# Kernel optimization log

Hardware: AMD Instinct MI355X
Metric: run time of the kernel (lower is better)

Reference implementation:

```python
import jax, jax.numpy as jnp
import numpy as np

N_PER_GROUP = 64
INPUT_DIM = 512
BATCH = 16384


def setup_inputs() -> dict:
    key = jax.random.key(0)
    k1, k2, k3 = jax.random.split(key, 3)
    x = jax.random.normal(k1, (BATCH, INPUT_DIM), dtype=jnp.float32)
    # xavier-uniform-ish prototypes
    prototype_vectors = jax.random.normal(k2, (2, N_PER_GROUP, INPUT_DIM), dtype=jnp.float32) * 0.05
    # mixture_fn = Linear(2*d, d)
    W_mix = jax.random.normal(k3, (INPUT_DIM, 2 * INPUT_DIM), dtype=jnp.float32) * (1.0 / np.sqrt(2 * INPUT_DIM))
    b_mix = jnp.zeros((INPUT_DIM,), dtype=jnp.float32)
    return {"x": x, "prototype_vectors": prototype_vectors, "W_mix": W_mix, "b_mix": b_mix}


def _mixed_prototypes(prototype_vectors, W_mix, b_mix):
    # Batched replacement of the nested j,l Python loop:
    # pair (j,l) -> concat(proto[0,j], proto[1,l]) -> Linear(2d -> d)
    n, d = prototype_vectors.shape[1], prototype_vectors.shape[2]
    g0 = jnp.broadcast_to(prototype_vectors[0][:, None, :], (n, n, d))  # [j,l,d]
    g1 = jnp.broadcast_to(prototype_vectors[1][None, :, :], (n, n, d))  # [j,l,d]
    pairs = jnp.concatenate([g0, g1], axis=-1).reshape(n * n, 2 * d)     # [n^2, 2d]
    return pairs @ W_mix.T + b_mix                                       # [n^2, d]


def reference(x, prototype_vectors, W_mix, b_mix):
    p = _mixed_prototypes(prototype_vectors, W_mix, b_mix)  # [P, d]
    # list_of_distances: pairwise squared Euclidean distance [B, P]
    xx = jnp.sum(x * x, axis=-1, keepdims=True)         # [B,1]
    pp = jnp.sum(p * p, axis=-1)[None, :]               # [1,P]
    return xx - 2.0 * (x @ p.T) + pp                    # [B,P]
```

## Files before the change

kernel.cpp:

```cpp
#include <hip/hip_runtime.h>
#include <hip/hip_bf16.h>

#define BATCH 16384
#define DIM   512
#define NPG   64
#define NPAIR 4096
#define NA    128

typedef float f32x4 __attribute__((ext_vector_type(4)));
typedef short s16x8 __attribute__((ext_vector_type(8)));

static __device__ __forceinline__ unsigned short f2bf(float f) {
    union { float f; unsigned u; } v; v.f = f;
    unsigned r = (v.u + 0x7FFFu + ((v.u >> 16) & 1u)) >> 16;
    return (unsigned short)r;
}

__global__ void k1_mixA(const float* __restrict__ proto, const float* __restrict__ W,
                        float* __restrict__ Af, unsigned short* __restrict__ Ab) {
    int gid = blockIdx.x * blockDim.x + threadIdx.x;
    int j = gid & (NA - 1);
    int d = gid >> 7;
    int koff = (j < NPG) ? 0 : DIM;
    const float4* pr = (const float4*)(proto + j * DIM);
    const float4* wr = (const float4*)(W + d * (2 * DIM) + koff);
    float a0 = 0.f, a1 = 0.f, a2 = 0.f, a3 = 0.f;
#pragma unroll 4
    for (int k4 = 0; k4 < DIM / 4; ++k4) {
        float4 p = pr[k4], w = wr[k4];
        a0 += p.x * w.x; a1 += p.y * w.y; a2 += p.z * w.z; a3 += p.w * w.w;
    }
    float a = (a0 + a1) + (a2 + a3);
    Af[j * DIM + d] = a;
    Ab[j * DIM + d] = f2bf(a);
}

__global__ void k2_pp(const float* __restrict__ Af, const float* __restrict__ bm,
                      float* __restrict__ pp) {
    int wave = (blockIdx.x * blockDim.x + threadIdx.x) >> 6;
    int lane = threadIdx.x & 63;
    int j = wave >> 6, l = wave & 63;
    const float4* r0 = (const float4*)(Af + j * DIM);
    const float4* r1 = (const float4*)(Af + (NPG + l) * DIM);
    const float4* bb = (const float4*)bm;
    float acc = 0.f;
#pragma unroll
    for (int i = 0; i < 2; ++i) {
        int idx = lane * 2 + i;
        float4 v0 = r0[idx], v1 = r1[idx], vb = bb[idx];
        float s;
        s = v0.x + v1.x + vb.x; acc += s * s;
        s = v0.y + v1.y + vb.y; acc += s * s;
        s = v0.z + v1.z + vb.z; acc += s * s;
        s = v0.w + v1.w + vb.w; acc += s * s;
    }
#pragma unroll
    for (int off = 32; off > 0; off >>= 1) acc += __shfl_xor(acc, off);
    if (lane == 0) pp[wave] = acc;
}

__global__ void k3_xxw(const float* __restrict__ x, const float* __restrict__ bm,
                       float* __restrict__ xx, float* __restrict__ w) {
    int wave = (blockIdx.x * blockDim.x + threadIdx.x) >> 6;
    int lane = threadIdx.x & 63;
    const float4* xr = (const float4*)(x + (size_t)wave * DIM);
    const float4* bb = (const float4*)bm;
    float axx = 0.f, aw = 0.f;
#pragma unroll
    for (int i = 0; i < 2; ++i) {
        int idx = lane * 2 + i;
        float4 v = xr[idx], vb = bb[idx];
        axx += v.x * v.x + v.y * v.y + v.z * v.z + v.w * v.w;
        aw  += v.x * vb.x + v.y * vb.y + v.z * vb.z + v.w * vb.w;
    }
#pragma unroll
    for (int off = 32; off > 0; off >>= 1) {
        axx += __shfl_xor(axx, off);
        aw  += __shfl_xor(aw, off);
    }
    if (lane == 0) { xx[wave] = axx; w[wave] = aw; }
}

__global__ void k4_gemm(const float* __restrict__ x, const unsigned short* __restrict__ Ab,
                        float* __restrict__ U) {
    int lane = threadIdx.x & 63;
    int wv = threadIdx.x >> 6;
    int m0 = blockIdx.x * 64 + wv * 16;
    int r = lane & 15, g = lane >> 4;
    f32x4 acc[8];
#pragma unroll
    for (int ct = 0; ct < 8; ++ct) acc[ct] = (f32x4){0.f, 0.f, 0.f, 0.f};
    const float* xrow = x + (size_t)(m0 + r) * DIM;
    for (int k0 = 0; k0 < DIM; k0 += 32) {
        int kb = k0 + g * 8;
        float4 xa = *(const float4*)(xrow + kb);
        float4 xb = *(const float4*)(xrow + kb + 4);
        s16x8 xf;
        xf[0] = (short)f2bf(xa.x); xf[1] = (short)f2bf(xa.y);
        xf[2] = (short)f2bf(xa.z); xf[3] = (short)f2bf(xa.w);
        xf[4] = (short)f2bf(xb.x); xf[5] = (short)f2bf(xb.y);
        xf[6] = (short)f2bf(xb.z); xf[7] = (short)f2bf(xb.w);
#pragma unroll
        for (int ct = 0; ct < 8; ++ct) {
            s16x8 bf = *(const s16x8*)(Ab + (ct * 16 + r) * DIM + kb);
            acc[ct] = __builtin_amdgcn_mfma_f32_16x16x32_bf16(xf, bf, acc[ct], 0, 0, 0);
        }
    }
#pragma unroll
    for (int ct = 0; ct < 8; ++ct)
#pragma unroll
        for (int rr = 0; rr < 4; ++rr)
            U[(size_t)(m0 + g * 4 + rr) * NA + ct * 16 + r] = acc[ct][rr];
}

__global__ void k5_out(const float* __restrict__ U, const float* __restrict__ xx,
                       const float* __restrict__ w, const float* __restrict__ pp,
                       float* __restrict__ out) {
    int b = blockIdx.x;
    int t = threadIdx.x;
    float base0 = xx[b] - 2.0f * w[b];
    const float* Ur = U + (size_t)b * NA;
    float* orow = out + (size_t)b * NPAIR;
#pragma unroll
    for (int i = 0; i < 4; ++i) {
        int idx = i * 1024 + t * 4;
        int j = idx >> 6, l = idx & 63;
        float uj = Ur[j];
        float4 v4 = *(const float4*)(Ur + NPG + l);
        float4 p4 = *(const float4*)(pp + idx);
        float base = base0 - 2.0f * uj;
        float4 o;
        o.x = base + p4.x - 2.0f * v4.x;
        o.y = base + p4.y - 2.0f * v4.y;
        o.z = base + p4.z - 2.0f * v4.z;
        o.w = base + p4.w - 2.0f * v4.w;
        *(float4*)(orow + idx) = o;
    }
}

extern "C" void kernel_launch(void* const* d_in, const int* in_sizes, int n_in,
                              void* d_out, int out_size, void* d_ws, size_t ws_size,
                              hipStream_t stream) {
    const float* x     = (const float*)d_in[0];
    const float* proto = (const float*)d_in[1];
    const float* Wmix  = (const float*)d_in[2];
    const float* bmix  = (const float*)d_in[3];
    float* out = (float*)d_out;

    float* ws = (float*)d_ws;
    float*          Af = ws;
    unsigned short* Ab = (unsigned short*)(ws + 65536);
    float*          pp = ws + 65536 + 32768;
    float*          xx = pp + NPAIR;
    float*          w  = xx + BATCH;
    float*          U  = w + BATCH;

    k1_mixA<<<256, 256, 0, stream>>>(proto, Wmix, Af, Ab);
    k2_pp  <<<1024, 256, 0, stream>>>(Af, bmix, pp);
    k3_xxw <<<4096, 256, 0, stream>>>(x, bmix, xx, w);
    k4_gemm<<<256, 256, 0, stream>>>(x, Ab, U);
    k5_out <<<BATCH, 256, 0, stream>>>(U, xx, w, pp, out);
}
```

Before: 106.8 us.

## Fuse row norms, bf16 GEMM and output expansion into one kernel

Merges the x-norm/bias-dot kernel, the MFMA GEMM and the output-expansion kernel into one kernel. Each 256-thread block handles 32 rows, keeps the 128-column U tile and the pp vector in shared memory, and writes the 4096-wide output rows directly. This removes the U/xx/w round trips through global memory, a second full read of x, and two launches. In exchange there are only 512 blocks, each writing a large output slab serially per row, which may limit the parallelism available for the store-bound phase.

```diff
diff --git a/kernel.cpp b/kernel.cpp
--- a/kernel.cpp
+++ b/kernel.cpp
@@ -6,6 +6,7 @@
 #define NPG   64
 #define NPAIR 4096
 #define NA    128
+#define ROWS  32
 
 typedef float f32x4 __attribute__((ext_vector_type(4)));
 typedef short s16x8 __attribute__((ext_vector_type(8)));
@@ -59,82 +60,89 @@
     if (lane == 0) pp[wave] = acc;
 }
 
-__global__ void k3_xxw(const float* __restrict__ x, const float* __restrict__ bm,
-                       float* __restrict__ xx, float* __restrict__ w) {
-    int wave = (blockIdx.x * blockDim.x + threadIdx.x) >> 6;
-    int lane = threadIdx.x & 63;
-    const float4* xr = (const float4*)(x + (size_t)wave * DIM);
-    const float4* bb = (const float4*)bm;
+__global__ void kc_fused(const float* __restrict__ x, const unsigned short* __restrict__ Ab,
+                         const float* __restrict__ bm, const float* __restrict__ pp,
+                         float* __restrict__ out) {
+    __shared__ float Ut[ROWS][NA];
+    __shared__ float pps[NPAIR];
+    __shared__ float xs[ROWS], wsum[ROWS];
+
+    int t = threadIdx.x;
+    int lane = t & 63;
+    int wv = t >> 6;
+    int r = lane & 15, g = lane >> 4;
+    int m0 = blockIdx.x * ROWS;
+    int rpair = wv >> 1;
+    int chalf = wv & 1;
+    int cbase = chalf * 64;
+
+#pragma unroll
+    for (int i = 0; i < 4; ++i)
+        ((float4*)pps)[i * 256 + t] = ((const float4*)pp)[i * 256 + t];
+
+    f32x4 acc[4];
+#pragma unroll
+    for (int ct = 0; ct < 4; ++ct) acc[ct] = (f32x4){0.f, 0.f, 0.f, 0.f};
+
+    const float* xrow = x + (size_t)(m0 + rpair * 16 + r) * DIM;
     float axx = 0.f, aw = 0.f;
-#pragma unroll
-    for (int i = 0; i < 2; ++i) {
-        int idx = lane * 2 + i;
-        float4 v = xr[idx], vb = bb[idx];
-        axx += v.x * v.x + v.y * v.y + v.z * v.z + v.w * v.w;
-        aw  += v.x * vb.x + v.y * vb.y + v.z * vb.z + v.w * vb.w;
-    }
-#pragma unroll
-    for (int off = 32; off > 0; off >>= 1) {
-        axx += __shfl_xor(axx, off);
-        aw  += __shfl_xor(aw, off);
-    }
-    if (lane == 0) { xx[wave] = axx; w[wave] = aw; }
-}
 
-__global__ void k4_gemm(const float* __restrict__ x, const unsigned short* __restrict__ Ab,
-                        float* __restrict__ U) {
-    int lane = threadIdx.x & 63;
-    int wv = threadIdx.x >> 6;
-    int m0 = blockIdx.x * 64 + wv * 16;
-    int r = lane & 15, g = lane >> 4;
-    f32x4 acc[8];
-#pragma unroll
-    for (int ct = 0; ct < 8; ++ct) acc[ct] = (f32x4){0.f, 0.f, 0.f, 0.f};
-    const float* xrow = x + (size_t)(m0 + r) * DIM;
     for (int k0 = 0; k0 < DIM; k0 += 32) {
         int kb = k0 + g * 8;
         float4 xa = *(const float4*)(xrow + kb);
         float4 xb = *(const float4*)(xrow + kb + 4);
+        if (chalf == 0) {
+            float4 b0 = *(const float4*)(bm + kb);
+            float4 b1 = *(const float4*)(bm + kb + 4);
+            axx += xa.x * xa.x + xa.y * xa.y + xa.z * xa.z + xa.w * xa.w
+                 + xb.x * xb.x + xb.y * xb.y + xb.z * xb.z + xb.w * xb.w;
+            aw  += xa.x * b0.x + xa.y * b0.y + xa.z * b0.z + xa.w * b0.w
+                 + xb.x * b1.x + xb.y * b1.y + xb.z * b1.z + xb.w * b1.w;
+        }
         s16x8 xf;
         xf[0] = (short)f2bf(xa.x); xf[1] = (short)f2bf(xa.y);
         xf[2] = (short)f2bf(xa.z); xf[3] = (short)f2bf(xa.w);
         xf[4] = (short)f2bf(xb.x); xf[5] = (short)f2bf(xb.y);
         xf[6] = (short)f2bf(xb.z); xf[7] = (short)f2bf(xb.w);
 #pragma unroll
-        for (int ct = 0; ct < 8; ++ct) {
-            s16x8 bf = *(const s16x8*)(Ab + (ct * 16 + r) * DIM + kb);
+        for (int ct = 0; ct < 4; ++ct) {
+            s16x8 bf = *(const s16x8*)(Ab + (size_t)(cbase + ct * 16 + r) * DIM + kb);
             acc[ct] = __builtin_amdgcn_mfma_f32_16x16x32_bf16(xf, bf, acc[ct], 0, 0, 0);
         }
     }
+
 #pragma unroll
-    for (int ct = 0; ct < 8; ++ct)
+    for (int ct = 0; ct < 4; ++ct)
 #pragma unroll
         for (int rr = 0; rr < 4; ++rr)
-            U[(size_t)(m0 + g * 4 + rr) * NA + ct * 16 + r] = acc[ct][rr];
-}
+            Ut[rpair * 16 + g * 4 + rr][cbase + ct * 16 + r] = acc[ct][rr];
 
-__global__ void k5_out(const float* __restrict__ U, const float* __restrict__ xx,
-                       const float* __restrict__ w, const float* __restrict__ pp,
-                       float* __restrict__ out) {
-    int b = blockIdx.x;
-    int t = threadIdx.x;
-    float base0 = xx[b] - 2.0f * w[b];
-    const float* Ur = U + (size_t)b * NA;
-    float* orow = out + (size_t)b * NPAIR;
+    if (chalf == 0) {
+        axx += __shfl_xor(axx, 16); axx += __shfl_xor(axx, 32);
+        aw  += __shfl_xor(aw, 16);  aw  += __shfl_xor(aw, 32);
+        if (g == 0) { xs[rpair * 16 + r] = axx; wsum[rpair * 16 + r] = aw; }
+    }
+    __syncthreads();
+
+    for (int rr = 0; rr < ROWS; ++rr) {
+        float base0 = xs[rr] - 2.0f * wsum[rr];
+        const float* Ur = Ut[rr];
+        float* orow = out + (size_t)(m0 + rr) * NPAIR;
 #pragma unroll
-    for (int i = 0; i < 4; ++i) {
-        int idx = i * 1024 + t * 4;
-        int j = idx >> 6, l = idx & 63;
-        float uj = Ur[j];
-        float4 v4 = *(const float4*)(Ur + NPG + l);
-        float4 p4 = *(const float4*)(pp + idx);
-        float base = base0 - 2.0f * uj;
-        float4 o;
-        o.x = base + p4.x - 2.0f * v4.x;
-        o.y = base + p4.y - 2.0f * v4.y;
-        o.z = base + p4.z - 2.0f * v4.z;
-        o.w = base + p4.w - 2.0f * v4.w;
-        *(float4*)(orow + idx) = o;
+        for (int i = 0; i < 4; ++i) {
+            int idx = (i * 256 + t) * 4;
+            int j = idx >> 6, l = idx & 63;
+            float uj = Ur[j];
+            float4 v4 = *(const float4*)(Ur + NPG + l);
+            float4 p4 = *(const float4*)(pps + idx);
+            float base = base0 - 2.0f * uj;
+            float4 o;
+            o.x = base + p4.x - 2.0f * v4.x;
+            o.y = base + p4.y - 2.0f * v4.y;
+            o.z = base + p4.z - 2.0f * v4.z;
+            o.w = base + p4.w - 2.0f * v4.w;
+            *(float4*)(orow + idx) = o;
+        }
     }
 }
 
@@ -151,13 +159,8 @@
     float*          Af = ws;
     unsigned short* Ab = (unsigned short*)(ws + 65536);
     float*          pp = ws + 65536 + 32768;
-    float*          xx = pp + NPAIR;
-    float*          w  = xx + BATCH;
-    float*          U  = w + BATCH;
 
-    k1_mixA<<<256, 256, 0, stream>>>(proto, Wmix, Af, Ab);
-    k2_pp  <<<1024, 256, 0, stream>>>(Af, bmix, pp);
-    k3_xxw <<<4096, 256, 0, stream>>>(x, bmix, xx, w);
-    k4_gemm<<<256, 256, 0, stream>>>(x, Ab, U);
-    k5_out <<<BATCH, 256, 0, stream>>>(U, xx, w, pp, out);
+    k1_mixA <<<256, 256, 0, stream>>>(proto, Wmix, Af, Ab);
+    k2_pp   <<<1024, 256, 0, stream>>>(Af, bmix, pp);
+    kc_fused<<<512, 256, 0, stream>>>(x, Ab, bmix, pp, out);
 }
```

New measurement: 139.9 us. 31.0% more time.

## Tile epilogue into 256x256 blocks and broadcast V columns via MFMA

Applied to the files above, without the earlier changes.

Replaces the per-row output kernel with a tiled epilogue. Each block handles 256 batch rows by 256 pairs, precomputes rb-2u terms in shared memory, and uses an MFMA with a one-hot -2 selector matrix to add the bf16 V values into the output tile. The GEMM now writes the U half in fp32 and the V half in bf16, and xx and w are merged into one per-row term. The aim is fewer, larger blocks and less redundant per-row U/pp traffic in the output-bound stage, at the cost of rounding V to bf16.

```diff
diff --git a/kernel.cpp b/kernel.cpp
--- a/kernel.cpp
+++ b/kernel.cpp
@@ -59,8 +59,8 @@
     if (lane == 0) pp[wave] = acc;
 }
 
-__global__ void k3_xxw(const float* __restrict__ x, const float* __restrict__ bm,
-                       float* __restrict__ xx, float* __restrict__ w) {
+__global__ void k3_rb(const float* __restrict__ x, const float* __restrict__ bm,
+                      float* __restrict__ rb) {
     int wave = (blockIdx.x * blockDim.x + threadIdx.x) >> 6;
     int lane = threadIdx.x & 63;
     const float4* xr = (const float4*)(x + (size_t)wave * DIM);
@@ -78,11 +78,11 @@
         axx += __shfl_xor(axx, off);
         aw  += __shfl_xor(aw, off);
     }
-    if (lane == 0) { xx[wave] = axx; w[wave] = aw; }
+    if (lane == 0) rb[wave] = axx - 2.0f * aw;
 }
 
 __global__ void k4_gemm(const float* __restrict__ x, const unsigned short* __restrict__ Ab,
-                        float* __restrict__ U) {
+                        float* __restrict__ Uf, unsigned short* __restrict__ Vb) {
     int lane = threadIdx.x & 63;
     int wv = threadIdx.x >> 6;
     int m0 = blockIdx.x * 64 + wv * 16;
@@ -102,39 +102,86 @@
         xf[6] = (short)f2bf(xb.z); xf[7] = (short)f2bf(xb.w);
 #pragma unroll
         for (int ct = 0; ct < 8; ++ct) {
-            s16x8 bf = *(const s16x8*)(Ab + (ct * 16 + r) * DIM + kb);
+            s16x8 bf = *(const s16x8*)(Ab + (size_t)(ct * 16 + r) * DIM + kb);
             acc[ct] = __builtin_amdgcn_mfma_f32_16x16x32_bf16(xf, bf, acc[ct], 0, 0, 0);
         }
     }
 #pragma unroll
-    for (int ct = 0; ct < 8; ++ct)
+    for (int ct = 0; ct < 4; ++ct)
 #pragma unroll
         for (int rr = 0; rr < 4; ++rr)
-            U[(size_t)(m0 + g * 4 + rr) * NA + ct * 16 + r] = acc[ct][rr];
-}
-
-__global__ void k5_out(const float* __restrict__ U, const float* __restrict__ xx,
-                       const float* __restrict__ w, const float* __restrict__ pp,
-                       float* __restrict__ out) {
-    int b = blockIdx.x;
+            Uf[(size_t)(m0 + g * 4 + rr) * 64 + ct * 16 + r] = acc[ct][rr];
+#pragma unroll
+    for (int ct = 4; ct < 8; ++ct)
+#pragma unroll
+        for (int rr = 0; rr < 4; ++rr)
+            Vb[(size_t)(m0 + g * 4 + rr) * 64 + (ct - 4) * 16 + r] = f2bf(acc[ct][rr]);
+}
+
+__global__ void kO_epilogue(const float* __restrict__ Uf, const unsigned short* __restrict__ Vb,
+                            const float* __restrict__ rb, const float* __restrict__ pp,
+                            float* __restrict__ out) {
+    __shared__ float rbU[4][256];
     int t = threadIdx.x;
-    float base0 = xx[b] - 2.0f * w[b];
-    const float* Ur = U + (size_t)b * NA;
-    float* orow = out + (size_t)b * NPAIR;
-#pragma unroll
-    for (int i = 0; i < 4; ++i) {
-        int idx = i * 1024 + t * 4;
-        int j = idx >> 6, l = idx & 63;
-        float uj = Ur[j];
-        float4 v4 = *(const float4*)(Ur + NPG + l);
-        float4 p4 = *(const float4*)(pp + idx);
-        float base = base0 - 2.0f * uj;
-        float4 o;
-        o.x = base + p4.x - 2.0f * v4.x;
-        o.y = base + p4.y - 2.0f * v4.y;
-        o.z = base + p4.z - 2.0f * v4.z;
-        o.w = base + p4.w - 2.0f * v4.w;
-        *(float4*)(orow + idx) = o;
+    int lane = t & 63;
+    int w = t >> 6;
+    int r = lane & 15, g = lane >> 4;
+    int col_blk = blockIdx.x & 15;
+    int row_blk = blockIdx.x >> 4;
+    int p0 = col_blk * 256;
+    int m0 = row_blk * 256;
+    int jbase = p0 >> 6;
+
+    {
+        float rbv = rb[m0 + t];
+        const float* urow = Uf + (size_t)(m0 + t) * 64 + jbase;
+#pragma unroll
+        for (int jj = 0; jj < 4; ++jj)
+            rbU[jj][t] = rbv - 2.0f * urow[jj];
+    }
+
+    s16x8 sf[4];
+#pragma unroll
+    for (int v = 0; v < 4; ++v) {
+        int pos = ((v & 1) << 4) + r;
+        int hit_g = pos >> 3;
+        int hit_e = pos & 7;
+#pragma unroll
+        for (int e = 0; e < 8; ++e)
+            sf[v][e] = (g == hit_g && e == hit_e) ? (short)0xC000 : (short)0;
+    }
+
+    f32x4 pp4[16];
+#pragma unroll
+    for (int mt = 0; mt < 16; ++mt)
+        pp4[mt] = *(const f32x4*)(pp + p0 + mt * 16 + g * 4);
+
+    __syncthreads();
+
+#pragma unroll
+    for (int bti = 0; bti < 4; ++bti) {
+        int bt = w * 4 + bti;
+        int brow = m0 + bt * 16 + r;
+        const unsigned short* vrow = Vb + (size_t)brow * 64;
+        s16x8 vb0 = *(const s16x8*)(vrow + g * 8);
+        s16x8 vb1 = *(const s16x8*)(vrow + 32 + g * 8);
+        float rbu0 = rbU[0][bt * 16 + r];
+        float rbu1 = rbU[1][bt * 16 + r];
+        float rbu2 = rbU[2][bt * 16 + r];
+        float rbu3 = rbU[3][bt * 16 + r];
+        float* obase = out + (size_t)brow * NPAIR + p0 + g * 4;
+#pragma unroll
+        for (int mt = 0; mt < 16; ++mt) {
+            int v = mt & 3;
+            float ru = (mt >> 2) == 0 ? rbu0 : (mt >> 2) == 1 ? rbu1 : (mt >> 2) == 2 ? rbu2 : rbu3;
+            f32x4 c;
+            c[0] = pp4[mt][0] + ru;
+            c[1] = pp4[mt][1] + ru;
+            c[2] = pp4[mt][2] + ru;
+            c[3] = pp4[mt][3] + ru;
+            c = __builtin_amdgcn_mfma_f32_16x16x32_bf16(sf[v], (v >> 1) ? vb1 : vb0, c, 0, 0, 0);
+            *(f32x4*)(obase + mt * 16) = c;
+        }
     }
 }
 
@@ -149,15 +196,15 @@
 
     float* ws = (float*)d_ws;
     float*          Af = ws;
-    unsigned short* Ab = (unsigned short*)(ws + 65536);
-    float*          pp = ws + 65536 + 32768;
-    float*          xx = pp + NPAIR;
-    float*          w  = xx + BATCH;
-    float*          U  = w + BATCH;
-
-    k1_mixA<<<256, 256, 0, stream>>>(proto, Wmix, Af, Ab);
-    k2_pp  <<<1024, 256, 0, stream>>>(Af, bmix, pp);
-    k3_xxw <<<4096, 256, 0, stream>>>(x, bmix, xx, w);
-    k4_gemm<<<256, 256, 0, stream>>>(x, Ab, U);
-    k5_out <<<BATCH, 256, 0, stream>>>(U, xx, w, pp, out);
-}
+    float*          pp = ws + 65536;
+    float*          rbv= ws + 69632;
+    float*          Uf = ws + 86016;
+    unsigned short* Ab = (unsigned short*)(ws + 86016 + 1048576);
+    unsigned short* Vb = Ab + 65536;
+
+    k1_mixA    <<<256, 256, 0, stream>>>(proto, Wmix, Af, Ab);
+    k2_pp      <<<1024, 256, 0, stream>>>(Af, bmix, pp);
+    k3_rb      <<<4096, 256, 0, stream>>>(x, bmix, rbv);
+    k4_gemm    <<<256, 256, 0, stream>>>(x, Ab, Uf, Vb);
+    kO_epilogue<<<1024, 256, 0, stream>>>(Uf, Vb, rbv, pp, out);
+}
```

Result: slower. 117.2 us (+9.7%).
